# Optimization experiments

Hardware: AMD Instinct MI355X
Metric: run time of the kernel (lower is better)

The kernel has to match this reference:

```python
import jax, jax.numpy as jnp
import numpy as np
from jax import lax

N, T, U, V = 32, 512, 100, 4096
BLANK = 0


def setup_inputs() -> dict:
    key = jax.random.key(0)
    k1, k2, k3, k4, k5 = jax.random.split(key, 5)
    encoder_out = jax.random.normal(k1, (N, T, V), dtype=jnp.float32)
    decoder_out = jax.random.normal(k2, (N, U + 1, V), dtype=jnp.float32)
    targets = jax.random.randint(k3, (N, U), 1, V)            # labels, never blank
    input_lengths = jax.random.randint(k4, (N,), T // 2, T + 1)
    target_lengths = jax.random.randint(k5, (N,), U // 2, U + 1)
    return {
        "encoder_out": encoder_out,
        "decoder_out": decoder_out,
        "targets": targets,
        "input_lengths": input_lengths,
        "target_lengths": target_lengths,
    }


def _logprob_single(enc, dec, y, in_len, tgt_len):
    # enc: (T, V)  dec: (U+1, V)  y: (U,)
    Um = y.shape[0]
    u_idx = jnp.arange(Um)
    # emit[t, u] = enc[t, y[u]] + dec[u, y[u]]  (cost of emitting label u+1 at time t)
    emit = enc[:, y] + dec[u_idx, y][None, :]          # (T, U)
    blank_e = enc[:, BLANK]                            # (T,)
    blank_d = dec[:, BLANK]                            # (U+1,)

    # t = 0 row: alpha[0, u] = sum_{k<u} emit[0, k]
    alpha0 = jnp.concatenate([jnp.zeros((1,), enc.dtype), jnp.cumsum(emit[0])])

    def row_step(alpha_prev, xs):
        be_prev, emit_t = xs
        # blank transition from row t-1 (same u)
        top = alpha_prev + be_prev + blank_d           # (U+1,)

        # label transition within row: alpha[u] = logaddexp(top[u], alpha[u-1] + emit_t[u-1])
        def u_step(carry, x):
            top_u, em = x
            a = jnp.logaddexp(top_u, carry + em)
            return a, a

        _, rest = lax.scan(u_step, top[0], (top[1:], emit_t))
        alpha = jnp.concatenate([top[:1], rest])
        return alpha, alpha

    _, rows = lax.scan(row_step, alpha0, (blank_e[:-1], emit[1:]))
    alphas = jnp.concatenate([alpha0[None, :], rows], axis=0)   # (T, U+1)

    # log p(y|x) = alpha[T-1, U] + enc[T-1, blank] + dec[U, blank] with true lengths
    return alphas[in_len - 1, tgt_len] + enc[in_len - 1, BLANK] + dec[tgt_len, BLANK]


def reference(encoder_out, decoder_out, targets, input_lengths, target_lengths):
    # reduction='none': returns per-utterance log p(y|x), shape (N,)
    return jax.vmap(_logprob_single)(encoder_out, decoder_out, targets,
                                     input_lengths, target_lengths)
```

## Files before the change

kernel.cpp:

```cpp
#include <hip/hip_runtime.h>

#define NB 32
#define TT 512
#define UU 100
#define UM 101
#define VV 4096
#define NEG (-1e30f)
#define WIN 64
#define L2E 1.4426950408889634f
#define LN2 0.6931471805599453f

__device__ __forceinline__ float vexp2(float x){ float r; asm("v_exp_f32 %0, %1" : "=v"(r) : "v"(x)); return r; }
__device__ __forceinline__ float vlog2(float x){ float r; asm("v_log_f32 %0, %1" : "=v"(r) : "v"(x)); return r; }

__device__ __forceinline__ float lae2(float a, float b) {
    float m  = fmaxf(a, b);
    float nd = fminf(a, b) - m;
    return m + vlog2(1.0f + vexp2(nd));
}

__global__ __launch_bounds__(1024, 1) void fused_k(
        const float* __restrict__ enc, const float* __restrict__ dec,
        const int* __restrict__ tgt, const int* __restrict__ ilen,
        const int* __restrict__ tlen, float* __restrict__ out) {
    __shared__ float em[2][WIN][128];
    __shared__ float blkL[864];
    __shared__ int   tgtL[UU];
    __shared__ float dvxL[UU];

    int n = blockIdx.x;
    int tid = threadIdx.x;
    int tin = ilen[n], tg = tlen[n];
    int dend = tin - 1 + tg;
    int E = (dend + WIN - 1) / WIN;
    const float* encn = enc + (size_t)n * TT * VV;

    for (int i = tid; i < 864; i += 1024)
        blkL[i] = (i >= 128 && i < 128 + TT) ? encn[(size_t)(i - 128) * VV] * L2E : NEG;
    if (tid < UU) {
        int y = tgt[n * UU + tid];
        tgtL[tid] = y;
        dvxL[tid] = dec[((size_t)n * UM + tid) * VV + y] * L2E;
    }
    __syncthreads();

    int wave = tid >> 6;
    int lane = tid & 63;

    auto FILLWIN = [&](int w, int baseDp) {
        int pid = tid - 64;
        float* emw = &em[w][0][0];
#pragma unroll
        for (int it = 0; it < 9; ++it) {
            int idx = pid + it * 960;
            if (idx < WIN * 128) {
                int dm = idx >> 7, u = idx & 127;
                int d = baseDp + dm + 1;
                int t = d - u;
                float val = NEG;
                if (u >= 1 && u <= tg && t >= 0 && t < tin)
                    val = fmaf(encn[(size_t)t * VV + tgtL[u - 1]], L2E, dvxL[u - 1]);
                emw[idx] = val;
            }
        }
    };

    if (wave != 0) FILLWIN(0, 0);

    int u0c = min(2 * lane, UM - 1), u1c = min(2 * lane + 1, UM - 1);
    float bd0 = dec[((size_t)n * UM + u0c) * VV] * L2E;
    float bd1 = dec[((size_t)n * UM + u1c) * VV] * L2E;
    int ib0 = 127 - 2 * lane;
    bool cap0 = (2 * lane == tg), cap1 = (2 * lane + 1 == tg);
    bool fx16 = (lane == 16), fx32 = (lane == 32), fx48 = (lane == 48);
    float a0 = (lane == 0) ? 0.0f : NEG;
    float a1 = NEG;
    float res = NEG;

    float Ae0[8], Ae1[8], Ab0[8], Ab1[8], Be0[8], Be1[8], Bb0[8], Bb1[8];

    auto REFILL = [&](float (&Re0)[8], float (&Re1)[8], float (&Rb0)[8], float (&Rb1)[8],
                      int j0, int dbase, const float* emb) {
#pragma unroll
        for (int k = 0; k < 8; ++k) {
            int dm = j0 + k;
            float2 ev = *(const float2*)(emb + dm * 128 + 2 * lane);
            int d = dbase + dm + 1;
            Re0[k] = ev.x; Re1[k] = ev.y;
            Rb0[k] = blkL[ib0 + d] + bd0;
            Rb1[k] = blkL[ib0 + d - 1] + bd1;
        }
        __builtin_amdgcn_sched_barrier(0);
    };

    auto STEPS = [&](float (&Re0)[8], float (&Re1)[8], float (&Rb0)[8], float (&Rb1)[8],
                     int j0, int dbase) {
#pragma unroll
        for (int k = 0; k < 8; ++k) {
            int dd = dbase + j0 + k + 1;
            int sh = __builtin_amdgcn_update_dpp(__float_as_int(NEG), __float_as_int(a1),
                                                 0x111, 0xF, 0xF, false);
            float s15 = __int_as_float(__builtin_amdgcn_readlane(__float_as_int(a1), 15));
            float s31 = __int_as_float(__builtin_amdgcn_readlane(__float_as_int(a1), 31));
            float s47 = __int_as_float(__builtin_amdgcn_readlane(__float_as_int(a1), 47));
            float l0 = __int_as_float(sh);
            l0 = fx16 ? s15 : l0;
            l0 = fx32 ? s31 : l0;
            l0 = fx48 ? s47 : l0;
            float bt0 = a0 + Rb0[k], et0 = l0 + Re0[k];
            float bt1 = a1 + Rb1[k], et1 = a0 + Re1[k];
            a0 = lae2(bt0, et0);
            a1 = lae2(bt1, et1);
            if (dd == dend) { if (cap0) res = a0; if (cap1) res = a1; }
        }
        __builtin_amdgcn_sched_barrier(0);
    };

    __syncthreads();

    for (int e = 0; e < E; ++e) {
        if (wave == 0) {
            int dbase = e * WIN;
            const float* emb = &em[e & 1][0][0];
            REFILL(Ae0, Ae1, Ab0, Ab1, 0, dbase, emb);
            REFILL(Be0, Be1, Bb0, Bb1, 8, dbase, emb);  STEPS(Ae0, Ae1, Ab0, Ab1, 0, dbase);
            REFILL(Ae0, Ae1, Ab0, Ab1, 16, dbase, emb); STEPS(Be0, Be1, Bb0, Bb1, 8, dbase);
            REFILL(Be0, Be1, Bb0, Bb1, 24, dbase, emb); STEPS(Ae0, Ae1, Ab0, Ab1, 16, dbase);
            REFILL(Ae0, Ae1, Ab0, Ab1, 32, dbase, emb); STEPS(Be0, Be1, Bb0, Bb1, 24, dbase);
            REFILL(Be0, Be1, Bb0, Bb1, 40, dbase, emb); STEPS(Ae0, Ae1, Ab0, Ab1, 32, dbase);
            REFILL(Ae0, Ae1, Ab0, Ab1, 48, dbase, emb); STEPS(Be0, Be1, Bb0, Bb1, 40, dbase);
            REFILL(Be0, Be1, Bb0, Bb1, 56, dbase, emb); STEPS(Ae0, Ae1, Ab0, Ab1, 48, dbase);
            STEPS(Be0, Be1, Bb0, Bb1, 56, dbase);
        } else {
            FILLWIN((e + 1) & 1, (e + 1) * WIN);
        }
        __syncthreads();
    }

    if (wave == 0 && (cap0 | cap1)) {
        float fin  = blkL[128 + tin - 1];
        float bdtg = dec[((size_t)n * UM + tg) * VV] * L2E;
        out[n] = (res + fin + bdtg) * LN2;
    }
}

extern "C" void kernel_launch(void* const* d_in, const int* in_sizes, int n_in,
                              void* d_out, int out_size, void* d_ws, size_t ws_size,
                              hipStream_t hs) {
    const float* enc  = (const float*)d_in[0];
    const float* dec  = (const float*)d_in[1];
    const int*   tgt  = (const int*)d_in[2];
    const int*   ilen = (const int*)d_in[3];
    const int*   tlen = (const int*)d_in[4];
    float* out = (float*)d_out;

    hipLaunchKernelGGL(fused_k, dim3(NB), dim3(1024), 0, hs,
                       enc, dec, tgt, ilen, tlen, out);
}
```

Measured before the change: 71.90 us.

## Spread emission gathers across producer blocks with global-memory flag handoff

Moves the gathering of emission log-probs out of the per-utterance block and into separate producer blocks, 11 per utterance, one per diagonal window. They write to a global workspace and signal readiness through atomic flags. The consumer wave spin-waits per window and reads registers straight from global memory with a wider 16-step prefetch. This spreads the scattered enc gathers across many CUs instead of 15 waves on one CU, at the cost of an extra clear kernel, global round-trips and spin-wait synchronization. It also relies on producer blocks being co-resident with the consumers to avoid deadlock.

```diff
diff --git a/kernel.cpp b/kernel.cpp
--- a/kernel.cpp
+++ b/kernel.cpp
@@ -7,6 +7,9 @@
 #define VV 4096
 #define NEG (-1e30f)
 #define WIN 64
+#define NWIN 11
+#define DST 720
+#define PW 16
 #define L2E 1.4426950408889634f
 #define LN2 0.6931471805599453f
 
@@ -19,73 +22,89 @@
     return m + vlog2(1.0f + vexp2(nd));
 }
 
-__global__ __launch_bounds__(1024, 1) void fused_k(
+__global__ void clear_k(int* __restrict__ flags) {
+    flags[threadIdx.x] = 0;
+}
+
+__global__ __launch_bounds__(256, 1) void fused_k(
         const float* __restrict__ enc, const float* __restrict__ dec,
         const int* __restrict__ tgt, const int* __restrict__ ilen,
-        const int* __restrict__ tlen, float* __restrict__ out) {
-    __shared__ float em[2][WIN][128];
+        const int* __restrict__ tlen,
+        float* __restrict__ st, int* __restrict__ flags, float* __restrict__ out) {
+    int bid = blockIdx.x;
+    int tid = threadIdx.x;
+
+    if (bid >= NB) {
+        int pb = bid - NB;
+        int n = pb / NWIN, w = pb % NWIN;
+        __shared__ int   tgtL[UU];
+        __shared__ float dvxL[UU];
+        if (tid < UU) {
+            int y = tgt[n * UU + tid];
+            tgtL[tid] = y;
+            dvxL[tid] = dec[((size_t)n * UM + tid) * VV + y] * L2E;
+        }
+        int tin = ilen[n], tg = tlen[n];
+        __syncthreads();
+        const float* encn = enc + (size_t)n * TT * VV;
+        float* F = st + ((size_t)n * DST + (size_t)(w * WIN + 1)) * 128;
+#pragma unroll
+        for (int it = 0; it < 32; ++it) {
+            int idx = tid + it * 256;
+            int dm = idx >> 7, u = idx & 127;
+            int d = w * WIN + 1 + dm;
+            int t = d - u;
+            float val = NEG;
+            if (u >= 1 && u <= tg && t >= 0 && t < tin)
+                val = fmaf(encn[(size_t)t * VV + tgtL[u - 1]], L2E, dvxL[u - 1]);
+            F[idx] = val;
+        }
+        __syncthreads();
+        if (tid == 0) {
+            __threadfence();
+            atomicExch(&flags[n * 16 + w], 1);
+        }
+        return;
+    }
+
+    int n = bid;
     __shared__ float blkL[864];
-    __shared__ int   tgtL[UU];
-    __shared__ float dvxL[UU];
+    const float* encn = enc + (size_t)n * TT * VV;
+    for (int i = tid; i < 864; i += 256)
+        blkL[i] = (i >= 128 && i < 128 + TT) ? encn[(size_t)(i - 128) * VV] * L2E : NEG;
+    __syncthreads();
+    if (tid >= 64) return;
+    int lane = tid;
 
-    int n = blockIdx.x;
-    int tid = threadIdx.x;
     int tin = ilen[n], tg = tlen[n];
     int dend = tin - 1 + tg;
-    int E = (dend + WIN - 1) / WIN;
-    const float* encn = enc + (size_t)n * TT * VV;
-
-    for (int i = tid; i < 864; i += 1024)
-        blkL[i] = (i >= 128 && i < 128 + TT) ? encn[(size_t)(i - 128) * VV] * L2E : NEG;
-    if (tid < UU) {
-        int y = tgt[n * UU + tid];
-        tgtL[tid] = y;
-        dvxL[tid] = dec[((size_t)n * UM + tid) * VV + y] * L2E;
-    }
-    __syncthreads();
-
-    int wave = tid >> 6;
-    int lane = tid & 63;
-
-    auto FILLWIN = [&](int w, int baseDp) {
-        int pid = tid - 64;
-        float* emw = &em[w][0][0];
-#pragma unroll
-        for (int it = 0; it < 9; ++it) {
-            int idx = pid + it * 960;
-            if (idx < WIN * 128) {
-                int dm = idx >> 7, u = idx & 127;
-                int d = baseDp + dm + 1;
-                int t = d - u;
-                float val = NEG;
-                if (u >= 1 && u <= tg && t >= 0 && t < tin)
-                    val = fmaf(encn[(size_t)t * VV + tgtL[u - 1]], L2E, dvxL[u - 1]);
-                emw[idx] = val;
-            }
-        }
-    };
-
-    if (wave != 0) FILLWIN(0, 0);
-
-    int u0c = min(2 * lane, UM - 1), u1c = min(2 * lane + 1, UM - 1);
-    float bd0 = dec[((size_t)n * UM + u0c) * VV] * L2E;
-    float bd1 = dec[((size_t)n * UM + u1c) * VV] * L2E;
+    int WC = (dend + WIN - 1) / WIN;
+    const float* decn = dec + (size_t)n * UM * VV;
+    float bd0 = decn[(size_t)min(2 * lane, UM - 1) * VV] * L2E;
+    float bd1 = decn[(size_t)min(2 * lane + 1, UM - 1) * VV] * L2E;
+    const float* sp = st + (size_t)n * DST * 128 + 2 * lane;
     int ib0 = 127 - 2 * lane;
     bool cap0 = (2 * lane == tg), cap1 = (2 * lane + 1 == tg);
     bool fx16 = (lane == 16), fx32 = (lane == 32), fx48 = (lane == 48);
     float a0 = (lane == 0) ? 0.0f : NEG;
     float a1 = NEG;
     float res = NEG;
+    int* flg = flags + n * 16;
 
-    float Ae0[8], Ae1[8], Ab0[8], Ab1[8], Be0[8], Be1[8], Bb0[8], Bb1[8];
+    float Ae0[PW], Ae1[PW], Ab0[PW], Ab1[PW];
+    float Be0[PW], Be1[PW], Bb0[PW], Bb1[PW];
 
-    auto REFILL = [&](float (&Re0)[8], float (&Re1)[8], float (&Rb0)[8], float (&Rb1)[8],
-                      int j0, int dbase, const float* emb) {
+    auto WAIT = [&](int w) {
+        if (lane == 0) { while (atomicAdd(&flg[w], 0) == 0) {} }
+        __threadfence();
+    };
+
+    auto REFILL = [&](float (&Re0)[PW], float (&Re1)[PW],
+                      float (&Rb0)[PW], float (&Rb1)[PW], int d0) {
 #pragma unroll
-        for (int k = 0; k < 8; ++k) {
-            int dm = j0 + k;
-            float2 ev = *(const float2*)(emb + dm * 128 + 2 * lane);
-            int d = dbase + dm + 1;
+        for (int k = 0; k < PW; ++k) {
+            int d = d0 + k;
+            float2 ev = *(const float2*)(sp + (size_t)d * 128);
             Re0[k] = ev.x; Re1[k] = ev.y;
             Rb0[k] = blkL[ib0 + d] + bd0;
             Rb1[k] = blkL[ib0 + d - 1] + bd1;
@@ -93,11 +112,11 @@
         __builtin_amdgcn_sched_barrier(0);
     };
 
-    auto STEPS = [&](float (&Re0)[8], float (&Re1)[8], float (&Rb0)[8], float (&Rb1)[8],
-                     int j0, int dbase) {
+    auto STEPS = [&](float (&Re0)[PW], float (&Re1)[PW],
+                     float (&Rb0)[PW], float (&Rb1)[PW], int d0) {
 #pragma unroll
-        for (int k = 0; k < 8; ++k) {
-            int dd = dbase + j0 + k + 1;
+        for (int k = 0; k < PW; ++k) {
+            int dd = d0 + k;
             int sh = __builtin_amdgcn_update_dpp(__float_as_int(NEG), __float_as_int(a1),
                                                  0x111, 0xF, 0xF, false);
             float s15 = __int_as_float(__builtin_amdgcn_readlane(__float_as_int(a1), 15));
@@ -116,30 +135,20 @@
         __builtin_amdgcn_sched_barrier(0);
     };
 
-    __syncthreads();
-
-    for (int e = 0; e < E; ++e) {
-        if (wave == 0) {
-            int dbase = e * WIN;
-            const float* emb = &em[e & 1][0][0];
-            REFILL(Ae0, Ae1, Ab0, Ab1, 0, dbase, emb);
-            REFILL(Be0, Be1, Bb0, Bb1, 8, dbase, emb);  STEPS(Ae0, Ae1, Ab0, Ab1, 0, dbase);
-            REFILL(Ae0, Ae1, Ab0, Ab1, 16, dbase, emb); STEPS(Be0, Be1, Bb0, Bb1, 8, dbase);
-            REFILL(Be0, Be1, Bb0, Bb1, 24, dbase, emb); STEPS(Ae0, Ae1, Ab0, Ab1, 16, dbase);
-            REFILL(Ae0, Ae1, Ab0, Ab1, 32, dbase, emb); STEPS(Be0, Be1, Bb0, Bb1, 24, dbase);
-            REFILL(Be0, Be1, Bb0, Bb1, 40, dbase, emb); STEPS(Ae0, Ae1, Ab0, Ab1, 32, dbase);
-            REFILL(Ae0, Ae1, Ab0, Ab1, 48, dbase, emb); STEPS(Be0, Be1, Bb0, Bb1, 40, dbase);
-            REFILL(Be0, Be1, Bb0, Bb1, 56, dbase, emb); STEPS(Ae0, Ae1, Ab0, Ab1, 48, dbase);
-            STEPS(Be0, Be1, Bb0, Bb1, 56, dbase);
-        } else {
-            FILLWIN((e + 1) & 1, (e + 1) * WIN);
-        }
-        __syncthreads();
+    WAIT(0);
+    REFILL(Ae0, Ae1, Ab0, Ab1, 1);
+    for (int w = 0; w < WC; ++w) {
+        int b = w * WIN;
+        REFILL(Be0, Be1, Bb0, Bb1, b + 17); STEPS(Ae0, Ae1, Ab0, Ab1, b + 1);
+        REFILL(Ae0, Ae1, Ab0, Ab1, b + 33); STEPS(Be0, Be1, Bb0, Bb1, b + 17);
+        REFILL(Be0, Be1, Bb0, Bb1, b + 49); STEPS(Ae0, Ae1, Ab0, Ab1, b + 33);
+        if (w + 1 < WC) WAIT(w + 1);
+        REFILL(Ae0, Ae1, Ab0, Ab1, b + 65); STEPS(Be0, Be1, Bb0, Bb1, b + 49);
     }
 
-    if (wave == 0 && (cap0 | cap1)) {
+    if (cap0 | cap1) {
         float fin  = blkL[128 + tin - 1];
-        float bdtg = dec[((size_t)n * UM + tg) * VV] * L2E;
+        float bdtg = decn[(size_t)tg * VV] * L2E;
         out[n] = (res + fin + bdtg) * LN2;
     }
 }
@@ -154,6 +163,10 @@
     const int*   tlen = (const int*)d_in[4];
     float* out = (float*)d_out;
 
-    hipLaunchKernelGGL(fused_k, dim3(NB), dim3(1024), 0, hs,
-                       enc, dec, tgt, ilen, tlen, out);
+    float* st    = (float*)d_ws;
+    int*   flags = (int*)(st + (size_t)NB * DST * 128);
+
+    hipLaunchKernelGGL(clear_k, dim3(1), dim3(NB * 16), 0, hs, flags);
+    hipLaunchKernelGGL(fused_k, dim3(NB + NB * NWIN), dim3(256), 0, hs,
+                       enc, dec, tgt, ilen, tlen, st, flags, out);
 }
```

Measured after the change: 96.86 us. 1.35x slower.

## Pack emit and blank terms into float4 LDS tiles, freeze finished cells

Applied to the files above, without the earlier changes.

The producer waves now precompute both the emit and the blank-transition terms per diagonal cell and store them as one float4 per lane in LDS, so the serial wave 0 does a single vector LDS load per step instead of a float2 load plus two blank lookups and adds. Cells beyond the input length get a zero blank term, so they hold their final value and the per-step result-capture compare can be dropped. Global loads in the fill are issued in a batch before use, and the fill is skipped on the last window. The cost is a doubled LDS window footprint and more fill work on the producer waves.

```diff
diff --git a/kernel.cpp b/kernel.cpp
--- a/kernel.cpp
+++ b/kernel.cpp
@@ -23,96 +23,97 @@
         const float* __restrict__ enc, const float* __restrict__ dec,
         const int* __restrict__ tgt, const int* __restrict__ ilen,
         const int* __restrict__ tlen, float* __restrict__ out) {
-    __shared__ float em[2][WIN][128];
+    __shared__ float4 em[2][WIN][64];
     __shared__ float blkL[864];
+    __shared__ float bdL[128];
     __shared__ int   tgtL[UU];
     __shared__ float dvxL[UU];
 
-    int n = blockIdx.x;
-    int tid = threadIdx.x;
+    int n = blockIdx.x, tid = threadIdx.x;
     int tin = ilen[n], tg = tlen[n];
     int dend = tin - 1 + tg;
     int E = (dend + WIN - 1) / WIN;
     const float* encn = enc + (size_t)n * TT * VV;
+    const float* decn = dec + (size_t)n * UM * VV;
 
     for (int i = tid; i < 864; i += 1024)
         blkL[i] = (i >= 128 && i < 128 + TT) ? encn[(size_t)(i - 128) * VV] * L2E : NEG;
+    if (tid < 128) bdL[tid] = (tid < UM) ? decn[(size_t)tid * VV] * L2E : 0.0f;
     if (tid < UU) {
         int y = tgt[n * UU + tid];
         tgtL[tid] = y;
-        dvxL[tid] = dec[((size_t)n * UM + tid) * VV + y] * L2E;
+        dvxL[tid] = decn[(size_t)tid * VV + y] * L2E;
     }
     __syncthreads();
 
-    int wave = tid >> 6;
-    int lane = tid & 63;
+    int wave = tid >> 6, lane = tid & 63;
 
-    auto FILLWIN = [&](int w, int baseDp) {
+    auto FILLWIN = [&](int w, int base) {
         int pid = tid - 64;
-        float* emw = &em[w][0][0];
+        float e0r[5], e1r[5];
 #pragma unroll
-        for (int it = 0; it < 9; ++it) {
+        for (int it = 0; it < 5; ++it) {
+            int idx = min(pid + it * 960, WIN * 64 - 1);
+            int dm = idx >> 6, L = idx & 63;
+            int d = base + 1 + dm;
+            int t0 = d - 2 * L, t1 = t0 - 1;
+            int tc0 = min(max(t0, 0), tin - 1), tc1 = min(max(t1, 0), tin - 1);
+            int uc0 = min(max(2 * L, 1), tg),   uc1 = min(2 * L + 1, tg);
+            e0r[it] = encn[(size_t)tc0 * VV + tgtL[uc0 - 1]];
+            e1r[it] = encn[(size_t)tc1 * VV + tgtL[uc1 - 1]];
+        }
+#pragma unroll
+        for (int it = 0; it < 5; ++it) {
             int idx = pid + it * 960;
-            if (idx < WIN * 128) {
-                int dm = idx >> 7, u = idx & 127;
-                int d = baseDp + dm + 1;
-                int t = d - u;
-                float val = NEG;
-                if (u >= 1 && u <= tg && t >= 0 && t < tin)
-                    val = fmaf(encn[(size_t)t * VV + tgtL[u - 1]], L2E, dvxL[u - 1]);
-                emw[idx] = val;
+            if (idx < WIN * 64) {
+                int dm = idx >> 6, L = idx & 63;
+                int d = base + 1 + dm;
+                int u0 = 2 * L, u1 = 2 * L + 1;
+                int t0 = d - u0, t1 = t0 - 1;
+                int uc0 = min(max(u0, 1), tg), uc1 = min(u1, tg);
+                bool ok0 = (u0 >= 1) & (u0 <= tg) & (t0 >= 0) & (t0 < tin);
+                bool ok1 = (u1 <= tg) & (t1 >= 0) & (t1 < tin);
+                float e0 = ok0 ? fmaf(e0r[it], L2E, dvxL[uc0 - 1]) : NEG;
+                float e1 = ok1 ? fmaf(e1r[it], L2E, dvxL[uc1 - 1]) : NEG;
+                float b0 = (t0 >= 1 && t0 < tin) ? blkL[128 + t0 - 1] + bdL[u0]
+                                                 : (t0 >= tin ? 0.0f : NEG);
+                float b1 = (t1 >= 1 && t1 < tin) ? blkL[128 + t1 - 1] + bdL[u1]
+                                                 : (t1 >= tin ? 0.0f : NEG);
+                em[w][dm][L] = make_float4(e0, b0, e1, b1);
             }
         }
     };
 
     if (wave != 0) FILLWIN(0, 0);
 
-    int u0c = min(2 * lane, UM - 1), u1c = min(2 * lane + 1, UM - 1);
-    float bd0 = dec[((size_t)n * UM + u0c) * VV] * L2E;
-    float bd1 = dec[((size_t)n * UM + u1c) * VV] * L2E;
-    int ib0 = 127 - 2 * lane;
-    bool cap0 = (2 * lane == tg), cap1 = (2 * lane + 1 == tg);
     bool fx16 = (lane == 16), fx32 = (lane == 32), fx48 = (lane == 48);
     float a0 = (lane == 0) ? 0.0f : NEG;
     float a1 = NEG;
-    float res = NEG;
+    float4 R0[8], R1[8];
 
-    float Ae0[8], Ae1[8], Ab0[8], Ab1[8], Be0[8], Be1[8], Bb0[8], Bb1[8];
-
-    auto REFILL = [&](float (&Re0)[8], float (&Re1)[8], float (&Rb0)[8], float (&Rb1)[8],
-                      int j0, int dbase, const float* emb) {
+    auto STEP = [&](float4 v) {
+        int sh = __builtin_amdgcn_update_dpp(__float_as_int(NEG), __float_as_int(a1),
+                                             0x111, 0xF, 0xF, false);
+        float s15 = __int_as_float(__builtin_amdgcn_readlane(__float_as_int(a1), 15));
+        float s31 = __int_as_float(__builtin_amdgcn_readlane(__float_as_int(a1), 31));
+        float s47 = __int_as_float(__builtin_amdgcn_readlane(__float_as_int(a1), 47));
+        float l0 = __int_as_float(sh);
+        l0 = fx16 ? s15 : l0;
+        l0 = fx32 ? s31 : l0;
+        l0 = fx48 ? s47 : l0;
+        float bt0 = a0 + v.y, et0 = l0 + v.x;
+        float bt1 = a1 + v.w, et1 = a0 + v.z;
+        a0 = lae2(bt0, et0);
+        a1 = lae2(bt1, et1);
+    };
+    auto LD8 = [&](float4 (&R)[8], const float4* emw, int j0) {
 #pragma unroll
-        for (int k = 0; k < 8; ++k) {
-            int dm = j0 + k;
-            float2 ev = *(const float2*)(emb + dm * 128 + 2 * lane);
-            int d = dbase + dm + 1;
-            Re0[k] = ev.x; Re1[k] = ev.y;
-            Rb0[k] = blkL[ib0 + d] + bd0;
-            Rb1[k] = blkL[ib0 + d - 1] + bd1;
-        }
+        for (int k = 0; k < 8; ++k) R[k] = emw[(size_t)(j0 + k) * 64 + lane];
         __builtin_amdgcn_sched_barrier(0);
     };
-
-    auto STEPS = [&](float (&Re0)[8], float (&Re1)[8], float (&Rb0)[8], float (&Rb1)[8],
-                     int j0, int dbase) {
+    auto ST8 = [&](float4 (&R)[8]) {
 #pragma unroll
-        for (int k = 0; k < 8; ++k) {
-            int dd = dbase + j0 + k + 1;
-            int sh = __builtin_amdgcn_update_dpp(__float_as_int(NEG), __float_as_int(a1),
-                                                 0x111, 0xF, 0xF, false);
-            float s15 = __int_as_float(__builtin_amdgcn_readlane(__float_as_int(a1), 15));
-            float s31 = __int_as_float(__builtin_amdgcn_readlane(__float_as_int(a1), 31));
-            float s47 = __int_as_float(__builtin_amdgcn_readlane(__float_as_int(a1), 47));
-            float l0 = __int_as_float(sh);
-            l0 = fx16 ? s15 : l0;
-            l0 = fx32 ? s31 : l0;
-            l0 = fx48 ? s47 : l0;
-            float bt0 = a0 + Rb0[k], et0 = l0 + Re0[k];
-            float bt1 = a1 + Rb1[k], et1 = a0 + Re1[k];
-            a0 = lae2(bt0, et0);
-            a1 = lae2(bt1, et1);
-            if (dd == dend) { if (cap0) res = a0; if (cap1) res = a1; }
-        }
+        for (int k = 0; k < 8; ++k) STEP(R[k]);
         __builtin_amdgcn_sched_barrier(0);
     };
 
@@ -120,27 +121,30 @@
 
     for (int e = 0; e < E; ++e) {
         if (wave == 0) {
-            int dbase = e * WIN;
-            const float* emb = &em[e & 1][0][0];
-            REFILL(Ae0, Ae1, Ab0, Ab1, 0, dbase, emb);
-            REFILL(Be0, Be1, Bb0, Bb1, 8, dbase, emb);  STEPS(Ae0, Ae1, Ab0, Ab1, 0, dbase);
-            REFILL(Ae0, Ae1, Ab0, Ab1, 16, dbase, emb); STEPS(Be0, Be1, Bb0, Bb1, 8, dbase);
-            REFILL(Be0, Be1, Bb0, Bb1, 24, dbase, emb); STEPS(Ae0, Ae1, Ab0, Ab1, 16, dbase);
-            REFILL(Ae0, Ae1, Ab0, Ab1, 32, dbase, emb); STEPS(Be0, Be1, Bb0, Bb1, 24, dbase);
-            REFILL(Be0, Be1, Bb0, Bb1, 40, dbase, emb); STEPS(Ae0, Ae1, Ab0, Ab1, 32, dbase);
-            REFILL(Ae0, Ae1, Ab0, Ab1, 48, dbase, emb); STEPS(Be0, Be1, Bb0, Bb1, 40, dbase);
-            REFILL(Be0, Be1, Bb0, Bb1, 56, dbase, emb); STEPS(Ae0, Ae1, Ab0, Ab1, 48, dbase);
-            STEPS(Be0, Be1, Bb0, Bb1, 56, dbase);
-        } else {
+            const float4* emw = &em[e & 1][0][0];
+            LD8(R0, emw, 0);
+            LD8(R1, emw, 8);  ST8(R0);
+            LD8(R0, emw, 16); ST8(R1);
+            LD8(R1, emw, 24); ST8(R0);
+            LD8(R0, emw, 32); ST8(R1);
+            LD8(R1, emw, 40); ST8(R0);
+            LD8(R0, emw, 48); ST8(R1);
+            LD8(R1, emw, 56); ST8(R0);
+            ST8(R1);
+        } else if (e + 1 < E) {
             FILLWIN((e + 1) & 1, (e + 1) * WIN);
         }
         __syncthreads();
     }
 
-    if (wave == 0 && (cap0 | cap1)) {
-        float fin  = blkL[128 + tin - 1];
-        float bdtg = dec[((size_t)n * UM + tg) * VV] * L2E;
-        out[n] = (res + fin + bdtg) * LN2;
+    if (wave == 0) {
+        bool cap0 = (2 * lane == tg), cap1 = (2 * lane + 1 == tg);
+        if (cap0 | cap1) {
+            float res = cap0 ? a0 : a1;
+            float fin = blkL[128 + tin - 1];
+            float bdtg = bdL[tg];
+            out[n] = (res + fin + bdtg) * LN2;
+        }
     }
 }
 
```

Result: slower. 89.78 us (+24.9%).

## Split emission gather into separate sorted-index gather kernel before DP

Applied to the files above, without the earlier changes.

Adds a per-utterance bitonic sort of target labels and a wide gather kernel, launched over 16x32 blocks, that reads enc[t, y] in sorted column order and writes a transposed (N, U, T) emission buffer to workspace. The DP kernel then fills its shared-memory diagonal windows from this contiguous buffer instead of doing scattered global gathers while the DP runs. It also pads the shared row stride to 130 and skips the unnecessary final window fill. The gather latency is moved onto many blocks at the cost of two extra kernel launches and a workspace round trip.

```diff
diff --git a/kernel.cpp b/kernel.cpp
--- a/kernel.cpp
+++ b/kernel.cpp
@@ -19,85 +19,143 @@
     return m + vlog2(1.0f + vexp2(nd));
 }
 
-__global__ __launch_bounds__(1024, 1) void fused_k(
+__global__ __launch_bounds__(128) void sort_k(const int* __restrict__ tgt,
+                                              int* __restrict__ sy,
+                                              int* __restrict__ su) {
+    __shared__ int ky[128], pu[128];
+    int n = blockIdx.x, tid = threadIdx.x;
+    ky[tid] = (tid < UU) ? tgt[n * UU + tid] : 0x7FFFFFFF;
+    pu[tid] = tid;
+    __syncthreads();
+    for (int k = 2; k <= 128; k <<= 1)
+        for (int j = k >> 1; j > 0; j >>= 1) {
+            int i = tid, ix = i ^ j;
+            if (ix > i) {
+                bool up = ((i & k) == 0);
+                int a = ky[i], b = ky[ix];
+                if ((a > b) == up) {
+                    ky[i] = b; ky[ix] = a;
+                    int tmp = pu[i]; pu[i] = pu[ix]; pu[ix] = tmp;
+                }
+            }
+            __syncthreads();
+        }
+    sy[n * 128 + tid] = ky[tid];
+    su[n * 128 + tid] = pu[tid];
+}
+
+__global__ __launch_bounds__(256) void gather_k(
+        const float* __restrict__ enc, const int* __restrict__ ilen,
+        const int* __restrict__ tlen, const int* __restrict__ sy,
+        const int* __restrict__ su, float* __restrict__ em) {
+    int tt = blockIdx.x, n = blockIdx.y;
+    int tin = ilen[n], tg = tlen[n];
+    int t0 = tt * 32;
+    if (t0 >= tin) return;
+    __shared__ float tile[32][104];
+    __shared__ int syL[128], suL[128];
+    int tid = threadIdx.x;
+    if (tid < 128) { syL[tid] = sy[n * 128 + tid]; suL[tid] = su[n * 128 + tid]; }
+    __syncthreads();
+    const float* encn = enc + (size_t)n * TT * VV;
+    int wave = tid >> 6, lane = tid & 63;
+
+    float v[16];
+#pragma unroll
+    for (int it = 0; it < 8; ++it) {
+        int t = t0 + wave * 8 + it;
+        bool tok = (t < tin);
+        int s1 = lane + 64;
+        int j0 = suL[lane];
+        int j1 = (s1 < 128) ? suL[s1] : 0;
+        v[2 * it]     = NEG;
+        v[2 * it + 1] = NEG;
+        if (tok && j0 < tg)              v[2 * it]     = encn[(size_t)t * VV + syL[lane]] * L2E;
+        if (tok && s1 < 100 && j1 < tg)  v[2 * it + 1] = encn[(size_t)t * VV + syL[s1]] * L2E;
+    }
+#pragma unroll
+    for (int it = 0; it < 8; ++it) {
+        int tl = wave * 8 + it;
+        int s1 = lane + 64;
+        tile[tl][suL[lane]] = v[2 * it];
+        if (s1 < 100) tile[tl][suL[s1]] = v[2 * it + 1];
+    }
+    __syncthreads();
+    for (int idx = tid; idx < UU * 32; idx += 256) {
+        int j = idx >> 5, tl = idx & 31;
+        em[((size_t)n * UU + j) * TT + t0 + tl] = tile[tl][j];
+    }
+}
+
+__global__ __launch_bounds__(1024, 1) void dp_k(
         const float* __restrict__ enc, const float* __restrict__ dec,
         const int* __restrict__ tgt, const int* __restrict__ ilen,
-        const int* __restrict__ tlen, float* __restrict__ out) {
-    __shared__ float em[2][WIN][128];
+        const int* __restrict__ tlen, const float* __restrict__ em,
+        float* __restrict__ out) {
+    __shared__ float emL[2][WIN][130];
     __shared__ float blkL[864];
-    __shared__ int   tgtL[UU];
     __shared__ float dvxL[UU];
 
-    int n = blockIdx.x;
-    int tid = threadIdx.x;
+    int n = blockIdx.x, tid = threadIdx.x;
     int tin = ilen[n], tg = tlen[n];
     int dend = tin - 1 + tg;
     int E = (dend + WIN - 1) / WIN;
     const float* encn = enc + (size_t)n * TT * VV;
+    const float* decn = dec + (size_t)n * UM * VV;
 
     for (int i = tid; i < 864; i += 1024)
         blkL[i] = (i >= 128 && i < 128 + TT) ? encn[(size_t)(i - 128) * VV] * L2E : NEG;
     if (tid < UU) {
         int y = tgt[n * UU + tid];
-        tgtL[tid] = y;
-        dvxL[tid] = dec[((size_t)n * UM + tid) * VV + y] * L2E;
-    }
-    __syncthreads();
-
-    int wave = tid >> 6;
-    int lane = tid & 63;
-
-    auto FILLWIN = [&](int w, int baseDp) {
-        int pid = tid - 64;
-        float* emw = &em[w][0][0];
-#pragma unroll
-        for (int it = 0; it < 9; ++it) {
-            int idx = pid + it * 960;
-            if (idx < WIN * 128) {
-                int dm = idx >> 7, u = idx & 127;
-                int d = baseDp + dm + 1;
-                int t = d - u;
-                float val = NEG;
-                if (u >= 1 && u <= tg && t >= 0 && t < tin)
-                    val = fmaf(encn[(size_t)t * VV + tgtL[u - 1]], L2E, dvxL[u - 1]);
-                emw[idx] = val;
-            }
+        dvxL[tid] = decn[(size_t)tid * VV + y] * L2E;
+    }
+    __syncthreads();
+
+    int wave = tid >> 6, lane = tid & 63;
+    const float* emn = em + (size_t)n * UU * TT;
+
+    auto FILLWIN = [&](int w, int base) {
+        for (int r = wave - 1; r < 128; r += 15) {
+            int u = (r < 100) ? (r + 1) : ((r == 100) ? 0 : r);
+            int t = base + 1 + lane - u;
+            float val = NEG;
+            if (r < 100 && r < tg && t >= 0 && t < tin)
+                val = emn[(size_t)r * TT + t] + dvxL[r];
+            emL[w][lane][u] = val;
         }
     };
 
     if (wave != 0) FILLWIN(0, 0);
 
-    int u0c = min(2 * lane, UM - 1), u1c = min(2 * lane + 1, UM - 1);
-    float bd0 = dec[((size_t)n * UM + u0c) * VV] * L2E;
-    float bd1 = dec[((size_t)n * UM + u1c) * VV] * L2E;
+    bool fx16 = (lane == 16), fx32 = (lane == 32), fx48 = (lane == 48);
+    bool cap0 = (2 * lane == tg), cap1 = (2 * lane + 1 == tg);
+    float bd0 = decn[(size_t)min(2 * lane, UM - 1) * VV] * L2E;
+    float bd1 = decn[(size_t)min(2 * lane + 1, UM - 1) * VV] * L2E;
     int ib0 = 127 - 2 * lane;
-    bool cap0 = (2 * lane == tg), cap1 = (2 * lane + 1 == tg);
-    bool fx16 = (lane == 16), fx32 = (lane == 32), fx48 = (lane == 48);
     float a0 = (lane == 0) ? 0.0f : NEG;
     float a1 = NEG;
     float res = NEG;
 
-    float Ae0[8], Ae1[8], Ab0[8], Ab1[8], Be0[8], Be1[8], Bb0[8], Bb1[8];
-
-    auto REFILL = [&](float (&Re0)[8], float (&Re1)[8], float (&Rb0)[8], float (&Rb1)[8],
-                      int j0, int dbase, const float* emb) {
+    float Re0[8], Re1[8], Rb0[8], Rb1[8], Se0[8], Se1[8], Sb0[8], Sb1[8];
+
+    auto REFILL = [&](float (&e0)[8], float (&e1)[8], float (&b0)[8], float (&b1)[8],
+                      const float* emb, int j0, int base) {
 #pragma unroll
         for (int k = 0; k < 8; ++k) {
-            int dm = j0 + k;
-            float2 ev = *(const float2*)(emb + dm * 128 + 2 * lane);
-            int d = dbase + dm + 1;
-            Re0[k] = ev.x; Re1[k] = ev.y;
-            Rb0[k] = blkL[ib0 + d] + bd0;
-            Rb1[k] = blkL[ib0 + d - 1] + bd1;
+            int dm = j0 + k, d = base + 1 + dm;
+            float2 ev = *(const float2*)(emb + dm * 130 + 2 * lane);
+            e0[k] = ev.x; e1[k] = ev.y;
+            b0[k] = blkL[ib0 + d] + bd0;
+            b1[k] = blkL[ib0 + d - 1] + bd1;
         }
         __builtin_amdgcn_sched_barrier(0);
     };
 
-    auto STEPS = [&](float (&Re0)[8], float (&Re1)[8], float (&Rb0)[8], float (&Rb1)[8],
-                     int j0, int dbase) {
+    auto STEPS = [&](float (&e0)[8], float (&e1)[8], float (&b0)[8], float (&b1)[8],
+                     int j0, int base) {
 #pragma unroll
         for (int k = 0; k < 8; ++k) {
-            int dd = dbase + j0 + k + 1;
+            int dd = base + 1 + j0 + k;
             int sh = __builtin_amdgcn_update_dpp(__float_as_int(NEG), __float_as_int(a1),
                                                  0x111, 0xF, 0xF, false);
             float s15 = __int_as_float(__builtin_amdgcn_readlane(__float_as_int(a1), 15));
@@ -107,8 +165,8 @@
             l0 = fx16 ? s15 : l0;
             l0 = fx32 ? s31 : l0;
             l0 = fx48 ? s47 : l0;
-            float bt0 = a0 + Rb0[k], et0 = l0 + Re0[k];
-            float bt1 = a1 + Rb1[k], et1 = a0 + Re1[k];
+            float bt0 = a0 + b0[k], et0 = l0 + e0[k];
+            float bt1 = a1 + b1[k], et1 = a0 + e1[k];
             a0 = lae2(bt0, et0);
             a1 = lae2(bt1, et1);
             if (dd == dend) { if (cap0) res = a0; if (cap1) res = a1; }
@@ -120,18 +178,18 @@
 
     for (int e = 0; e < E; ++e) {
         if (wave == 0) {
-            int dbase = e * WIN;
-            const float* emb = &em[e & 1][0][0];
-            REFILL(Ae0, Ae1, Ab0, Ab1, 0, dbase, emb);
-            REFILL(Be0, Be1, Bb0, Bb1, 8, dbase, emb);  STEPS(Ae0, Ae1, Ab0, Ab1, 0, dbase);
-            REFILL(Ae0, Ae1, Ab0, Ab1, 16, dbase, emb); STEPS(Be0, Be1, Bb0, Bb1, 8, dbase);
-            REFILL(Be0, Be1, Bb0, Bb1, 24, dbase, emb); STEPS(Ae0, Ae1, Ab0, Ab1, 16, dbase);
-            REFILL(Ae0, Ae1, Ab0, Ab1, 32, dbase, emb); STEPS(Be0, Be1, Bb0, Bb1, 24, dbase);
-            REFILL(Be0, Be1, Bb0, Bb1, 40, dbase, emb); STEPS(Ae0, Ae1, Ab0, Ab1, 32, dbase);
-            REFILL(Ae0, Ae1, Ab0, Ab1, 48, dbase, emb); STEPS(Be0, Be1, Bb0, Bb1, 40, dbase);
-            REFILL(Be0, Be1, Bb0, Bb1, 56, dbase, emb); STEPS(Ae0, Ae1, Ab0, Ab1, 48, dbase);
-            STEPS(Be0, Be1, Bb0, Bb1, 56, dbase);
-        } else {
+            int base = e * WIN;
+            const float* emb = &emL[e & 1][0][0];
+            REFILL(Re0, Re1, Rb0, Rb1, emb, 0, base);
+            REFILL(Se0, Se1, Sb0, Sb1, emb, 8, base);  STEPS(Re0, Re1, Rb0, Rb1, 0, base);
+            REFILL(Re0, Re1, Rb0, Rb1, emb, 16, base); STEPS(Se0, Se1, Sb0, Sb1, 8, base);
+            REFILL(Se0, Se1, Sb0, Sb1, emb, 24, base); STEPS(Re0, Re1, Rb0, Rb1, 16, base);
+            REFILL(Re0, Re1, Rb0, Rb1, emb, 32, base); STEPS(Se0, Se1, Sb0, Sb1, 24, base);
+            REFILL(Se0, Se1, Sb0, Sb1, emb, 40, base); STEPS(Re0, Re1, Rb0, Rb1, 32, base);
+            REFILL(Re0, Re1, Rb0, Rb1, emb, 48, base); STEPS(Se0, Se1, Sb0, Sb1, 40, base);
+            REFILL(Se0, Se1, Sb0, Sb1, emb, 56, base); STEPS(Re0, Re1, Rb0, Rb1, 48, base);
+            STEPS(Se0, Se1, Sb0, Sb1, 56, base);
+        } else if (e + 1 < E) {
             FILLWIN((e + 1) & 1, (e + 1) * WIN);
         }
         __syncthreads();
@@ -139,7 +197,7 @@
 
     if (wave == 0 && (cap0 | cap1)) {
         float fin  = blkL[128 + tin - 1];
-        float bdtg = dec[((size_t)n * UM + tg) * VV] * L2E;
+        float bdtg = decn[(size_t)tg * VV] * L2E;
         out[n] = (res + fin + bdtg) * LN2;
     }
 }
@@ -154,6 +212,13 @@
     const int*   tlen = (const int*)d_in[4];
     float* out = (float*)d_out;
 
-    hipLaunchKernelGGL(fused_k, dim3(NB), dim3(1024), 0, hs,
-                       enc, dec, tgt, ilen, tlen, out);
-}
+    float* em = (float*)d_ws;
+    int*   sy = (int*)(em + (size_t)NB * UU * TT);
+    int*   su = sy + NB * 128;
+
+    hipLaunchKernelGGL(sort_k,   dim3(NB), dim3(128), 0, hs, tgt, sy, su);
+    hipLaunchKernelGGL(gather_k, dim3(16, NB), dim3(256), 0, hs,
+                       enc, ilen, tlen, sy, su, em);
+    hipLaunchKernelGGL(dp_k,     dim3(NB), dim3(1024), 0, hs,
+                       enc, dec, tgt, ilen, tlen, em, out);
+}
```

Result: slower. 78.04 us (+8.5%).
